# Optimization experiments

Hardware: AMD Instinct MI355X
Metric: run time of the kernel (lower is better)

The kernel has to match this reference:

```python
import jax, jax.numpy as jnp
import numpy as np

jax.config.update("jax_enable_x64", True)  # gaus_fit runs in float64, matching torch .double()

STAB_NB = 1e-15


def _gaus_fit(x):
    """Weighted Gaussian regression. x: (bn, x_len, col_len), values > 0."""
    col_len = x.shape[-1]
    col = jnp.arange(col_len, dtype=jnp.float64)          # (col_len,)
    y = x.astype(jnp.float64)
    y2 = y * y
    lny = jnp.log(y)
    y2l = y2 * lny
    x1, x2, x3, x4 = col, col**2, col**3, col**4
    s_y2    = jnp.sum(y2, -1)
    s_xy2   = jnp.sum(x1 * y2, -1)
    s_x2y2  = jnp.sum(x2 * y2, -1)
    s_x3y2  = jnp.sum(x3 * y2, -1)
    s_x4y2  = jnp.sum(x4 * y2, -1)
    s_y2l   = jnp.sum(y2l, -1)
    s_xy2l  = jnp.sum(x1 * y2l, -1)
    s_x2y2l = jnp.sum(x2 * y2l, -1)
    b_num = (s_x2y2**2 * s_xy2l - s_y2 * s_x4y2 * s_xy2l + s_xy2 * s_x4y2 * s_y2l
             + s_y2 * s_x3y2 * s_x2y2l - s_x2y2 * s_x3y2 * s_y2l - s_xy2 * s_x2y2 * s_x2y2l)
    c_num = (s_x2y2l * s_xy2**2 - s_xy2l * s_xy2 * s_x2y2 - s_x3y2 * s_y2l * s_xy2
             + s_y2l * s_x2y2**2 - s_y2 * s_x2y2l * s_x2y2 + s_y2 * s_x3y2 * s_xy2l)
    # clamp |c_num| away from zero (sign(0)*STAB -> 0, same as torch.sign)
    c_num = jnp.where(jnp.abs(c_num) < STAB_NB, jnp.sign(c_num) * STAB_NB, c_num)
    mu = -b_num / (2.0 * c_num)
    c_din = (s_x4y2 * s_xy2**2 - 2.0 * s_xy2 * s_x2y2 * s_x3y2 + s_x2y2**3
             - s_y2 * s_x4y2 * s_x2y2 + s_y2 * s_x3y2**2)
    sigma = -0.5 * c_din / c_num
    sigma = jnp.where(sigma < 1.0, 1.0, sigma)
    return mu.astype(jnp.float32), sigma.astype(jnp.float32)


def _newton_sol(g_mean, g_sigma, w_comp):
    """Solve (H_pair + diag(1/sigma)) x = mean/sigma via dense inverse (faithful to source)."""
    n = g_mean.shape[1]
    w = w_comp.astype(jnp.float32)[0]
    main = jnp.concatenate([2.0 * w[None], 4.0 * w * jnp.ones(n - 2, jnp.float32), 2.0 * w[None]])
    off = -2.0 * w * jnp.ones(n - 1, jnp.float32)
    hess_pair = jnp.diag(main) + jnp.diag(off, 1) + jnp.diag(off, -1)   # (n, n)
    sig_rev = 1.0 / g_sigma                                              # (bn, n)
    hess = hess_pair[None, :, :] + jnp.eye(n, dtype=jnp.float32) * sig_rev[:, :, None]
    hess_inv = jnp.linalg.inv(hess)                                      # (bn, n, n)
    p = g_mean * sig_rev
    return jnp.einsum('bij,bj->bi', hess_inv, p)


def setup_inputs() -> dict:
    key = jax.random.key(0)
    k1, _ = jax.random.split(key)
    x = jax.random.normal(k1, (32, 1024, 512), dtype=jnp.float32)  # (BN, X_LEN, COL_LEN) logits
    w_comp = jnp.ones((1,), jnp.float32) * 1e-05                   # learned CRF weight
    return {"x": x, "w_comp": w_comp}


def reference(x, w_comp):
    # softmax over column (depth) axis
    p = jax.nn.softmax(x, axis=-1)
    # normalize_prob: min-max to [0,1] then +0.001
    pmin = jnp.min(p, -1, keepdims=True)
    pmax = jnp.max(p, -1, keepdims=True)
    pn = (p - pmin) / (pmax - pmin) + 0.001
    mu, sigma = _gaus_fit(pn)
    return _newton_sol(mu, sigma, w_comp)  # (BN, X_LEN), tr_flag=True path
```

## Files before the change

kernel.cpp:

```cpp
#include <hip/hip_runtime.h>
#include <hip/hip_bf16.h>
#include <math.h>

#define BN 32
#define XLEN 1024
#define COLS 512
#define ROWS (BN * XLEN)
#define STAB 1e-15

typedef float v2f __attribute__((ext_vector_type(2)));

#define HW_EXP2(x) __builtin_amdgcn_exp2f(x)
#define HW_LOG2(x) __builtin_amdgcn_logf(x)
#define HW_RCP(x)  __builtin_amdgcn_rcpf(x)

template <int CTRL>
__device__ __forceinline__ float dpp_rot_f32(float v) {
  return __int_as_float(__builtin_amdgcn_mov_dpp(
      __float_as_int(v), CTRL, 0xF, 0xF, false));
}
template <int CTRL>
__device__ __forceinline__ double dpp_rot_f64(double v) {
  const unsigned long long u = __double_as_longlong(v);
  const int lo = __builtin_amdgcn_mov_dpp((int)(u & 0xFFFFFFFFull),
                                          CTRL, 0xF, 0xF, false);
  const int hi = __builtin_amdgcn_mov_dpp((int)(u >> 32),
                                          CTRL, 0xF, 0xF, false);
  return __longlong_as_double(((unsigned long long)(unsigned)hi << 32) |
                              (unsigned)lo);
}
#define ROR8 0x128
#define ROR4 0x124
#define ROR2 0x122
#define ROR1 0x121

__device__ __forceinline__ float dpp_max16_f32(float v) {
  v = fmaxf(v, dpp_rot_f32<ROR8>(v));
  v = fmaxf(v, dpp_rot_f32<ROR4>(v));
  v = fmaxf(v, dpp_rot_f32<ROR2>(v));
  v = fmaxf(v, dpp_rot_f32<ROR1>(v));
  return v;
}
__device__ __forceinline__ float dpp_min16_f32(float v) {
  v = fminf(v, dpp_rot_f32<ROR8>(v));
  v = fminf(v, dpp_rot_f32<ROR4>(v));
  v = fminf(v, dpp_rot_f32<ROR2>(v));
  v = fminf(v, dpp_rot_f32<ROR1>(v));
  return v;
}
__device__ __forceinline__ double dpp_sum16_f64(double v) {
  v += dpp_rot_f64<ROR8>(v);
  v += dpp_rot_f64<ROR4>(v);
  v += dpp_rot_f64<ROR2>(v);
  v += dpp_rot_f64<ROR1>(v);
  return v;
}

__global__ __launch_bounds__(256) void gaus_fit_kernel(
    const float* __restrict__ x, float* __restrict__ mu_out,
    float* __restrict__ sig_out) {
  const int lane = threadIdx.x & 63;
  const int wid  = threadIdx.x >> 6;
  const int sub  = lane & 15;
  const int row  = blockIdx.x * 16 + wid * 4 + (lane >> 4);

  const v2f* rp2 = (const v2f*)(x + (size_t)row * COLS);
  v2f ve[16];
#pragma unroll
  for (int j = 0; j < 8; ++j) {
    ve[2 * j]     = rp2[32 * j + 2 * sub];
    ve[2 * j + 1] = rp2[32 * j + 2 * sub + 1];
  }

  v2f mx2 = ve[0], xn2 = ve[0];
#pragma unroll
  for (int k = 1; k < 16; ++k) {
    mx2 = __builtin_elementwise_max(mx2, ve[k]);
    xn2 = __builtin_elementwise_min(xn2, ve[k]);
  }
  const float mx = dpp_max16_f32(fmaxf(mx2.x, mx2.y));
  const float xn = dpp_min16_f32(fminf(xn2.x, xn2.y));

  const float LOG2E = 1.44269504089f;
  const float mxs  = mx * LOG2E;
  const float emin = HW_EXP2(fmaf(xn, LOG2E, -mxs));
  const float CA   = 1.0f / (1.0f - emin);
  const float CB   = fmaf(-emin, CA, 0.001f);
  const v2f L2E2 = {LOG2E, LOG2E};
  const v2f NMXS = {-mxs, -mxs};
  const v2f CA2 = {CA, CA}, CB2 = {CB, CB};

  const float bb = (float)(4 * sub) * (1.0f / 512.0f);
  v2f u0 = {0, 0}, u1 = {0, 0}, u2 = {0, 0}, u3 = {0, 0}, u4 = {0, 0};
  v2f w0 = {0, 0}, w1 = {0, 0}, w2 = {0, 0};

#define GF_PAIR(j, h)                                                         \
  {                                                                           \
    const int   k   = 2 * (j) + (h);                                          \
    const float off = (float)(64 * (j) + 2 * (h)) * (1.0f / 512.0f);          \
    const v2f xh = {bb + off, bb + off + 0.001953125f};                       \
    const v2f xs = __builtin_elementwise_fma(ve[k], L2E2, NMXS);              \
    v2f e;                                                                    \
    e.x = HW_EXP2(xs.x);                                                      \
    e.y = HW_EXP2(xs.y);                                                      \
    const v2f pn = __builtin_elementwise_fma(e, CA2, CB2);                    \
    v2f l2;                                                                   \
    l2.x = HW_LOG2(pn.x);                                                     \
    l2.y = HW_LOG2(pn.y);                                                     \
    const v2f y2  = pn * pn;                                                  \
    const v2f y2l = y2 * l2;                                                  \
    const v2f x2  = xh * xh;                                                  \
    const v2f x3  = x2 * xh;                                                  \
    const v2f x4  = x2 * x2;                                                  \
    u0 += y2;                                                                 \
    u1 = __builtin_elementwise_fma(xh, y2, u1);                               \
    u2 = __builtin_elementwise_fma(x2, y2, u2);                               \
    u3 = __builtin_elementwise_fma(x3, y2, u3);                               \
    u4 = __builtin_elementwise_fma(x4, y2, u4);                               \
    w0 += y2l;                                                                \
    w1 = __builtin_elementwise_fma(xh, y2l, w1);                              \
    w2 = __builtin_elementwise_fma(x2, y2l, w2);                              \
  }

#pragma unroll
  for (int j = 0; j < 8; ++j) {
    GF_PAIR(j, 0)
    GF_PAIR(j, 1)
  }
#undef GF_PAIR

  const double d0 = dpp_sum16_f64((double)u0.x + (double)u0.y);
  const double d1 = dpp_sum16_f64((double)u1.x + (double)u1.y);
  const double d2 = dpp_sum16_f64((double)u2.x + (double)u2.y);
  const double d3 = dpp_sum16_f64((double)u3.x + (double)u3.y);
  const double d4 = dpp_sum16_f64((double)u4.x + (double)u4.y);
  const double e0 = dpp_sum16_f64((double)w0.x + (double)w0.y);
  const double e1 = dpp_sum16_f64((double)w1.x + (double)w1.y);
  const double e2 = dpp_sum16_f64((double)w2.x + (double)w2.y);

  if (sub == 0) {
    const double LN2D = 0.6931471805599453;
    const double s_y2    = d0;
    const double s_xy2   = d1 * 512.0;
    const double s_x2y2  = d2 * 262144.0;
    const double s_x3y2  = d3 * 134217728.0;
    const double s_x4y2  = d4 * 68719476736.0;
    const double s_y2l   = e0 * LN2D;
    const double s_xy2l  = (e1 * 512.0) * LN2D;
    const double s_x2y2l = (e2 * 262144.0) * LN2D;
    const double A2 = s_x2y2 * s_x2y2;
    double b_num = A2 * s_xy2l - s_y2 * s_x4y2 * s_xy2l
                 + s_xy2 * s_x4y2 * s_y2l + s_y2 * s_x3y2 * s_x2y2l
                 - s_x2y2 * s_x3y2 * s_y2l - s_xy2 * s_x2y2 * s_x2y2l;
    double c_num = s_x2y2l * s_xy2 * s_xy2 - s_xy2l * s_xy2 * s_x2y2
                 - s_x3y2 * s_y2l * s_xy2 + s_y2l * A2
                 - s_y2 * s_x2y2l * s_x2y2 + s_y2 * s_x3y2 * s_xy2l;
    if (fabs(c_num) < STAB) {
      c_num = (c_num > 0.0) ? STAB : ((c_num < 0.0) ? -STAB : 0.0);
    }
    const double mu = -b_num / (2.0 * c_num);
    const double c_din = s_x4y2 * s_xy2 * s_xy2
                       - 2.0 * s_xy2 * s_x2y2 * s_x3y2 + s_x2y2 * A2
                       - s_y2 * s_x4y2 * s_x2y2 + s_y2 * s_x3y2 * s_x3y2;
    double sigma = -0.5 * c_din / c_num;
    if (sigma < 1.0) sigma = 1.0;
    mu_out[row]  = (float)mu;
    sig_out[row] = (float)sigma;
  }
}

__global__ __launch_bounds__(1024) void pcr_solve_kernel(
    const float* __restrict__ mu, const float* __restrict__ sigma,
    const float* __restrict__ w_comp, float* __restrict__ out) {
  __shared__ float A[2][XLEN], B[2][XLEN], C[2][XLEN], D[2][XLEN];
  const int i = threadIdx.x;
  const int g = blockIdx.x * XLEN + i;

  const float w = w_comp[0];
  const float offf  = -2.0f * w;
  const float mainw = (i == 0 || i == XLEN - 1) ? (2.0f * w) : (4.0f * w);
  const float sr = 1.0f / sigma[g];
  const float bf = mainw + sr;
  const float df = mu[g] * sr;

  A[0][i] = (i == 0) ? 0.0f : offf;
  C[0][i] = (i == XLEN - 1) ? 0.0f : offf;
  B[0][i] = bf;
  D[0][i] = df;
  __syncthreads();

  int cur = 0;
  for (int s = 1; s < XLEN; s <<= 1) {
    const float ai = A[cur][i], bi = B[cur][i], ci = C[cur][i], di = D[cur][i];
    float am = 0.0f, cm = 0.0f, dm = 0.0f, rm = 0.0f;
    float ap = 0.0f, cp = 0.0f, dp = 0.0f, rp = 0.0f;
    if (i >= s) {
      am = A[cur][i - s]; cm = C[cur][i - s]; dm = D[cur][i - s];
      rm = HW_RCP(B[cur][i - s]);
    }
    if (i + s < XLEN) {
      ap = A[cur][i + s]; cp = C[cur][i + s]; dp = D[cur][i + s];
      rp = HW_RCP(B[cur][i + s]);
    }
    const float k1 = ai * rm;
    const float k2 = ci * rp;
    const float nb = bi - k1 * cm - k2 * ap;
    const float nd = di - k1 * dm - k2 * dp;
    const int nxt = cur ^ 1;
    A[nxt][i] = -k1 * am;
    C[nxt][i] = -k2 * cp;
    B[nxt][i] = nb;
    D[nxt][i] = nd;
    __syncthreads();
    cur = nxt;
  }

  out[g] = D[cur][i] / B[cur][i];
}

extern "C" void kernel_launch(void* const* d_in, const int* in_sizes, int n_in,
                              void* d_out, int out_size, void* d_ws, size_t ws_size,
                              hipStream_t stream) {
  const float* x      = (const float*)d_in[0];
  const float* w_comp = (const float*)d_in[1];
  float* out = (float*)d_out;

  float* mu_ws  = (float*)d_ws;
  float* sig_ws = mu_ws + ROWS;

  gaus_fit_kernel<<<ROWS / 16, 256, 0, stream>>>(x, mu_ws, sig_ws);
  pcr_solve_kernel<<<BN, XLEN, 0, stream>>>(mu_ws, sig_ws, w_comp, out);
}
```

Measured before the change: 24.27 us.

## Fuse Gaussian fit and PCR solve into one kernel with per-batch atomic counters

Merges the two launches into one persistent-style kernel. The first BN blocks spin on a per-batch atomic counter until all 64 producer blocks for that batch have written mu and sigma, then run the PCR tridiagonal solve with 256 threads each handling 4 rows. The aim is to remove the second kernel launch gap and overlap each batch's solve with the fit of later batches. It adds a memset launch, spin-wait blocks that occupy CUs, and deadlock risk if the consumer blocks are scheduled before their producers can run.

Result: slower. 94.41 us (+288.9%).

```diff
diff --git a/kernel.cpp b/kernel.cpp
--- a/kernel.cpp
+++ b/kernel.cpp
@@ -56,13 +56,84 @@
   return v;
 }
 
-__global__ __launch_bounds__(256) void gaus_fit_kernel(
-    const float* __restrict__ x, float* __restrict__ mu_out,
-    float* __restrict__ sig_out) {
+__global__ __launch_bounds__(256) void surf_fused_kernel(
+    const float* __restrict__ x, const float* __restrict__ w_comp,
+    float* __restrict__ mu_ws, float* __restrict__ sig_ws,
+    unsigned* __restrict__ cnt, float* __restrict__ out) {
+  __shared__ float As[XLEN], Bs[XLEN], Cs[XLEN], Ds[XLEN];
+
+  if (blockIdx.x < BN) {
+    const int batch = blockIdx.x;
+    if (threadIdx.x == 0) {
+      while (__hip_atomic_load(&cnt[batch], __ATOMIC_ACQUIRE,
+                               __HIP_MEMORY_SCOPE_AGENT) < 64u) {
+        __builtin_amdgcn_s_sleep(32);
+      }
+    }
+    __syncthreads();
+    __threadfence();
+
+    const int base = batch * XLEN;
+    const float w = w_comp[0];
+    const float offf = -2.0f * w;
+    const int t = threadIdx.x;
+#pragma unroll
+    for (int q = 0; q < 4; ++q) {
+      const int i = t + 256 * q;
+      const float sr = 1.0f / sig_ws[base + i];
+      const float mainw = (i == 0 || i == XLEN - 1) ? (2.0f * w) : (4.0f * w);
+      As[i] = (i == 0) ? 0.0f : offf;
+      Cs[i] = (i == XLEN - 1) ? 0.0f : offf;
+      Bs[i] = mainw + sr;
+      Ds[i] = mu_ws[base + i] * sr;
+    }
+    __syncthreads();
+
+    for (int s = 1; s < XLEN; s <<= 1) {
+      float na[4], nb[4], nc[4], nd[4];
+#pragma unroll
+      for (int q = 0; q < 4; ++q) {
+        const int i = t + 256 * q;
+        const float ai = As[i], bi = Bs[i], ci = Cs[i], di = Ds[i];
+        float am = 0.0f, cm = 0.0f, dm = 0.0f, rm = 0.0f;
+        float ap = 0.0f, cp = 0.0f, dp = 0.0f, rp = 0.0f;
+        if (i >= s) {
+          am = As[i - s]; cm = Cs[i - s]; dm = Ds[i - s];
+          rm = HW_RCP(Bs[i - s]);
+        }
+        if (i + s < XLEN) {
+          ap = As[i + s]; cp = Cs[i + s]; dp = Ds[i + s];
+          rp = HW_RCP(Bs[i + s]);
+        }
+        const float k1 = ai * rm;
+        const float k2 = ci * rp;
+        nb[q] = bi - k1 * cm - k2 * ap;
+        nd[q] = di - k1 * dm - k2 * dp;
+        na[q] = -k1 * am;
+        nc[q] = -k2 * cp;
+      }
+      __syncthreads();
+#pragma unroll
+      for (int q = 0; q < 4; ++q) {
+        const int i = t + 256 * q;
+        As[i] = na[q]; Bs[i] = nb[q]; Cs[i] = nc[q]; Ds[i] = nd[q];
+      }
+      __syncthreads();
+    }
+
+#pragma unroll
+    for (int q = 0; q < 4; ++q) {
+      const int i = t + 256 * q;
+      out[base + i] = Ds[i] / Bs[i];
+    }
+    return;
+  }
+
+  const int bid  = blockIdx.x - BN;
   const int lane = threadIdx.x & 63;
   const int wid  = threadIdx.x >> 6;
   const int sub  = lane & 15;
-  const int row  = blockIdx.x * 16 + wid * 4 + (lane >> 4);
+  const int row  = bid * 16 + wid * 4 + (lane >> 4);
 
   const v2f* rp2 = (const v2f*)(x + (size_t)row * COLS);
   v2f ve[16];
@@ -164,58 +235,15 @@
                        - s_y2 * s_x4y2 * s_x2y2 + s_y2 * s_x3y2 * s_x3y2;
     double sigma = -0.5 * c_din / c_num;
     if (sigma < 1.0) sigma = 1.0;
-    mu_out[row]  = (float)mu;
-    sig_out[row] = (float)sigma;
-  }
-}
-
-__global__ __launch_bounds__(1024) void pcr_solve_kernel(
-    const float* __restrict__ mu, const float* __restrict__ sigma,
-    const float* __restrict__ w_comp, float* __restrict__ out) {
-  __shared__ float A[2][XLEN], B[2][XLEN], C[2][XLEN], D[2][XLEN];
-  const int i = threadIdx.x;
-  const int g = blockIdx.x * XLEN + i;
-
-  const float w = w_comp[0];
-  const float offf  = -2.0f * w;
-  const float mainw = (i == 0 || i == XLEN - 1) ? (2.0f * w) : (4.0f * w);
-  const float sr = 1.0f / sigma[g];
-  const float bf = mainw + sr;
-  const float df = mu[g] * sr;
-
-  A[0][i] = (i == 0) ? 0.0f : offf;
-  C[0][i] = (i == XLEN - 1) ? 0.0f : offf;
-  B[0][i] = bf;
-  D[0][i] = df;
+    mu_ws[row]  = (float)mu;
+    sig_ws[row] = (float)sigma;
+  }
+
   __syncthreads();
-
-  int cur = 0;
-  for (int s = 1; s < XLEN; s <<= 1) {
-    const float ai = A[cur][i], bi = B[cur][i], ci = C[cur][i], di = D[cur][i];
-    float am = 0.0f, cm = 0.0f, dm = 0.0f, rm = 0.0f;
-    float ap = 0.0f, cp = 0.0f, dp = 0.0f, rp = 0.0f;
-    if (i >= s) {
-      am = A[cur][i - s]; cm = C[cur][i - s]; dm = D[cur][i - s];
-      rm = HW_RCP(B[cur][i - s]);
-    }
-    if (i + s < XLEN) {
-      ap = A[cur][i + s]; cp = C[cur][i + s]; dp = D[cur][i + s];
-      rp = HW_RCP(B[cur][i + s]);
-    }
-    const float k1 = ai * rm;
-    const float k2 = ci * rp;
-    const float nb = bi - k1 * cm - k2 * ap;
-    const float nd = di - k1 * dm - k2 * dp;
-    const int nxt = cur ^ 1;
-    A[nxt][i] = -k1 * am;
-    C[nxt][i] = -k2 * cp;
-    B[nxt][i] = nb;
-    D[nxt][i] = nd;
-    __syncthreads();
-    cur = nxt;
-  }
-
-  out[g] = D[cur][i] / B[cur][i];
+  if (threadIdx.x == 0) {
+    __threadfence();
+    atomicAdd(&cnt[bid >> 6], 1u);
+  }
 }
 
 extern "C" void kernel_launch(void* const* d_in, const int* in_sizes, int n_in,
@@ -227,7 +255,9 @@
 
   float* mu_ws  = (float*)d_ws;
   float* sig_ws = mu_ws + ROWS;
-
-  gaus_fit_kernel<<<ROWS / 16, 256, 0, stream>>>(x, mu_ws, sig_ws);
-  pcr_solve_kernel<<<BN, XLEN, 0, stream>>>(mu_ws, sig_ws, w_comp, out);
-}
+  unsigned* cnt = (unsigned*)(sig_ws + ROWS);
+
+  hipMemsetAsync((void*)cnt, 0, BN * sizeof(unsigned), stream);
+  surf_fused_kernel<<<BN + ROWS / 16, 256, 0, stream>>>(
+      x, w_comp, mu_ws, sig_ws, cnt, out);
+}
```
